# Performance work log

Measured on AMD Instinct MI355X. Metric: run time of the kernel, lower is better.

The kernel has to match this reference:

```python
import math
import jax, jax.numpy as jnp
import numpy as np

Q_MAX = 127.0  # 2**(8-1) - 1 for n_bits=8
SCALE_EPS = 1e-5


def _hadamard_matrix(n):
    H = np.array([[1.0]], dtype=np.float32)
    while H.shape[0] < n:
        H = np.block([[H, H], [H, -H]])
    return jnp.asarray(H)


def quantize_per_channel_absmax(w):
    # per output-channel absmax quantize-dequantize (torch weight per_channel)
    scales = jnp.clip(jnp.max(jnp.abs(w), axis=-1, keepdims=True) / Q_MAX, SCALE_EPS, None)
    return jnp.round(w / scales) * scales


def quantize_per_token_absmax(x):
    # per-token (last-dim) absmax quantize-dequantize
    scales = jnp.clip(jnp.max(jnp.abs(x), axis=-1, keepdims=True) / Q_MAX, SCALE_EPS, None)
    return jnp.round(x / scales) * scales


def setup_inputs() -> dict:
    key = jax.random.key(0)
    k1, k2, k3 = jax.random.split(key, 3)
    B, S, D_IN, D_OUT = 2, 2048, 4096, 4096
    x = jax.random.normal(k1, (B, S, D_IN), dtype=jnp.float32)
    # weight quantized at __init__ time (per_channel, 8-bit), as in the wrapper
    weight = quantize_per_channel_absmax(
        jax.random.normal(k2, (D_OUT, D_IN), dtype=jnp.float32) * (1.0 / math.sqrt(D_IN)))
    bias = jax.random.normal(k3, (D_OUT,), dtype=jnp.float32)
    return {"x": x, "weight": weight, "bias": bias, "had_dim": 64}


def reference(x, weight, bias, had_dim):
    # --- online_partial_had, K == 1 path ---
    B, S, D = x.shape
    n_groups = D // had_dim
    H = _hadamard_matrix(n_groups).astype(x.dtype)
    xr = x.reshape(-1, n_groups, had_dim)  # (B*S, G, had_dim)
    # hadamard_transform along the group axis, scale = 1/sqrt(G)
    xr = jnp.einsum('hg,bgd->bhd', H, xr) * (1.0 / math.sqrt(n_groups))
    x = xr.reshape(B, S, D)
    # --- per-token absmax activation quant ---
    x = quantize_per_token_absmax(x)
    # --- linear with (already quantized) weight ---
    return jnp.einsum('bsd,od->bso', x, weight) + bias
```

## Files before the change

### kernel.cpp

```cpp
#include <hip/hip_runtime.h>

#define M_DIM 4096
#define N_DIM 4096
#define K_DIM 4096

typedef __attribute__((ext_vector_type(4))) int i32x4;
typedef __attribute__((ext_vector_type(16))) int i32x16;

typedef __attribute__((address_space(1))) const void GV;
typedef __attribute__((address_space(3))) void LV;

__global__ __launch_bounds__(256) void prequant_kernel(const float* __restrict__ x,
                                                       const float* __restrict__ w,
                                                       char* __restrict__ xq,
                                                       char* __restrict__ wq,
                                                       float* __restrict__ sx,
                                                       float* __restrict__ sw) {
  const int wave = threadIdx.x >> 6;
  const int lane = threadIdx.x & 63;

  if (blockIdx.x >= 1024) {
    const int row = (blockIdx.x - 1024) * 4 + wave;
    const float* wp = w + (size_t)row * 4096;
    float4 v[16];
#pragma unroll
    for (int c = 0; c < 16; ++c) v[c] = *(const float4*)(wp + c * 256 + lane * 4);
    float amax = 0.f;
#pragma unroll
    for (int c = 0; c < 16; ++c)
      amax = fmaxf(amax, fmaxf(fmaxf(fabsf(v[c].x), fabsf(v[c].y)),
                               fmaxf(fabsf(v[c].z), fabsf(v[c].w))));
#pragma unroll
    for (int off = 32; off >= 1; off >>= 1) amax = fmaxf(amax, __shfl_xor(amax, off, 64));
    amax = fmaxf(amax, 1e-30f);
    const float inv = 127.0f / amax;
    char* op = wq + (size_t)row * 4096;
#pragma unroll
    for (int c = 0; c < 16; ++c) {
      char4 o;
      o.x = (char)rintf(v[c].x * inv);
      o.y = (char)rintf(v[c].y * inv);
      o.z = (char)rintf(v[c].z * inv);
      o.w = (char)rintf(v[c].w * inv);
      *(char4*)(op + c * 256 + lane * 4) = o;
    }
    if (lane == 0) sw[row] = amax * (1.0f / 127.0f);
    return;
  }

  const int tok = blockIdx.x * 4 + wave;
  const int gs = lane >> 4;
  const int q = lane & 15;
  const float* xp = x + (size_t)tok * 4096;

  float4 v[16];
#pragma unroll
  for (int gl = 0; gl < 16; ++gl)
    v[gl] = *(const float4*)(xp + (gl * 4 + gs) * 64 + q * 4);

#pragma unroll
  for (int s = 1; s < 16; s <<= 1) {
#pragma unroll
    for (int i = 0; i < 16; ++i) {
      if ((i & s) == 0) {
        float4 a = v[i], b = v[i | s];
        v[i].x = a.x + b.x; v[i].y = a.y + b.y; v[i].z = a.z + b.z; v[i].w = a.w + b.w;
        v[i | s].x = a.x - b.x; v[i | s].y = a.y - b.y;
        v[i | s].z = a.z - b.z; v[i | s].w = a.w - b.w;
      }
    }
  }
#pragma unroll
  for (int st = 0; st < 2; ++st) {
    const int L = 16 << st;
    const bool hi = (lane & L) != 0;
#pragma unroll
    for (int i = 0; i < 16; ++i) {
      float4 t;
      t.x = __shfl_xor(v[i].x, L, 64);
      t.y = __shfl_xor(v[i].y, L, 64);
      t.z = __shfl_xor(v[i].z, L, 64);
      t.w = __shfl_xor(v[i].w, L, 64);
      if (hi) {
        v[i].x = t.x - v[i].x; v[i].y = t.y - v[i].y;
        v[i].z = t.z - v[i].z; v[i].w = t.w - v[i].w;
      } else {
        v[i].x += t.x; v[i].y += t.y; v[i].z += t.z; v[i].w += t.w;
      }
    }
  }

  float amax = 0.f;
#pragma unroll
  for (int i = 0; i < 16; ++i) {
    v[i].x *= 0.125f; v[i].y *= 0.125f; v[i].z *= 0.125f; v[i].w *= 0.125f;
    amax = fmaxf(amax, fmaxf(fmaxf(fabsf(v[i].x), fabsf(v[i].y)),
                             fmaxf(fabsf(v[i].z), fabsf(v[i].w))));
  }
#pragma unroll
  for (int off = 32; off >= 1; off >>= 1) amax = fmaxf(amax, __shfl_xor(amax, off, 64));

  const float s = fmaxf(amax * (1.0f / 127.0f), 1e-5f);
  const float inv = 1.0f / s;

  char* op = xq + (size_t)tok * 4096;
#pragma unroll
  for (int gl = 0; gl < 16; ++gl) {
    char4 o;
    o.x = (char)rintf(v[gl].x * inv);
    o.y = (char)rintf(v[gl].y * inv);
    o.z = (char)rintf(v[gl].z * inv);
    o.w = (char)rintf(v[gl].w * inv);
    *(char4*)(op + (gl * 4 + gs) * 64 + q * 4) = o;
  }
  if (lane == 0) sx[tok] = s;
}

__global__ __launch_bounds__(512, 2) void gemm_i8(const char* __restrict__ A,
                                                  const char* __restrict__ B,
                                                  const float* __restrict__ sx,
                                                  const float* __restrict__ sw,
                                                  const float* __restrict__ bias,
                                                  float* __restrict__ C) {
  __shared__ __align__(16) char sm[65536];

  const int tid = threadIdx.x;
  const int lane = tid & 63;
  const int wave = tid >> 6;
  const int wm = wave >> 2;
  const int wn = wave & 3;
  const int m32 = lane & 31;
  const int half = lane >> 5;

  const int bid = blockIdx.x;
  const int cx = bid & 7, ii = bid >> 3;
  const int bm = (cx & 3) * 4 + (ii >> 3);
  const int bn = (cx >> 2) * 8 + (ii & 7);

  const int strow = tid >> 1;
  const int stseg = ((tid & 1) ^ ((tid >> 3) & 1)) << 4;
  const char* gA = A + (size_t)(bm * 256 + strow) * K_DIM + stseg;
  const char* gB = B + (size_t)(bn * 256 + strow) * K_DIM + stseg;

  auto lof = [&](int row) { return row * 32 + ((half ^ ((row >> 2) & 1)) << 4); };
  const int aoff0 = lof(wm * 128 + 0 + m32);
  const int aoff1 = lof(wm * 128 + 32 + m32);
  const int aoff2 = lof(wm * 128 + 64 + m32);
  const int aoff3 = lof(wm * 128 + 96 + m32);
  const int boff0 = 8192 + lof(wn * 64 + 0 + m32);
  const int boff1 = 8192 + lof(wn * 64 + 32 + m32);

  i32x16 acc[4][2];
#pragma unroll
  for (int i = 0; i < 4; ++i)
#pragma unroll
    for (int j = 0; j < 2; ++j)
#pragma unroll
      for (int r = 0; r < 16; ++r) acc[i][j][r] = 0;

#pragma unroll
  for (int s = 0; s < 3; ++s) {
    char* ld = sm + s * 16384 + (tid << 4);
    const size_t ko = (size_t)s * 32;
    __builtin_amdgcn_global_load_lds((GV*)(gA + ko), (LV*)ld, 16, 0, 0);
    __builtin_amdgcn_global_load_lds((GV*)(gB + ko), (LV*)(ld + 8192), 16, 0, 0);
  }
  asm volatile("s_waitcnt vmcnt(4)" ::: "memory");
  __builtin_amdgcn_s_barrier();

#define KTILE(T, DOSTAGE, TAILWAIT)                                                   \
  {                                                                                   \
    const char* bufp = sm + ((T) & 3) * 16384;                                        \
    if (DOSTAGE) {                                                                    \
      char* ld = sm + (((T) + 3) & 3) * 16384 + (tid << 4);                           \
      const size_t ko = (size_t)((T) + 3) * 32;                                       \
      __builtin_amdgcn_global_load_lds((GV*)(gA + ko), (LV*)ld, 16, 0, 0);            \
      __builtin_amdgcn_global_load_lds((GV*)(gB + ko), (LV*)(ld + 8192), 16, 0, 0);   \
    }                                                                                 \
    const i32x4 a0 = *(const i32x4*)(bufp + aoff0);                                   \
    const i32x4 a1 = *(const i32x4*)(bufp + aoff1);                                   \
    const i32x4 a2 = *(const i32x4*)(bufp + aoff2);                                   \
    const i32x4 a3 = *(const i32x4*)(bufp + aoff3);                                   \
    const i32x4 b0 = *(const i32x4*)(bufp + boff0);                                   \
    const i32x4 b1 = *(const i32x4*)(bufp + boff1);                                   \
    __builtin_amdgcn_s_barrier();                                                     \
    asm volatile("s_waitcnt lgkmcnt(0)" ::: "memory");                                \
    __builtin_amdgcn_sched_barrier(0);                                                \
    __builtin_amdgcn_s_setprio(1);                                                    \
    acc[0][0] = __builtin_amdgcn_mfma_i32_32x32x32_i8(a0, b0, acc[0][0], 0, 0, 0);    \
    acc[0][1] = __builtin_amdgcn_mfma_i32_32x32x32_i8(a0, b1, acc[0][1], 0, 0, 0);    \
    acc[1][0] = __builtin_amdgcn_mfma_i32_32x32x32_i8(a1, b0, acc[1][0], 0, 0, 0);    \
    acc[1][1] = __builtin_amdgcn_mfma_i32_32x32x32_i8(a1, b1, acc[1][1], 0, 0, 0);    \
    acc[2][0] = __builtin_amdgcn_mfma_i32_32x32x32_i8(a2, b0, acc[2][0], 0, 0, 0);    \
    acc[2][1] = __builtin_amdgcn_mfma_i32_32x32x32_i8(a2, b1, acc[2][1], 0, 0, 0);    \
    acc[3][0] = __builtin_amdgcn_mfma_i32_32x32x32_i8(a3, b0, acc[3][0], 0, 0, 0);    \
    acc[3][1] = __builtin_amdgcn_mfma_i32_32x32x32_i8(a3, b1, acc[3][1], 0, 0, 0);    \
    __builtin_amdgcn_s_setprio(0);                                                    \
    asm volatile("s_waitcnt " TAILWAIT ::: "memory");                                 \
    __builtin_amdgcn_s_barrier();                                                     \
  }

#pragma unroll 1
  for (int t = 0; t < 125; ++t) {
    KTILE(t, 1, "vmcnt(4)");
  }
  KTILE(125, 0, "vmcnt(2)");
  KTILE(126, 0, "vmcnt(0)");
  KTILE(127, 0, "vmcnt(0)");
#undef KTILE

  const int col0 = bn * 256 + wn * 64 + m32;
  const float swv0 = sw[col0];
  const float swv1 = sw[col0 + 32];
  const float bv0 = bias[col0];
  const float bv1 = bias[col0 + 32];

#pragma unroll
  for (int fm = 0; fm < 4; ++fm) {
    const int rbase = bm * 256 + wm * 128 + fm * 32 + 4 * half;
    float sxv[16];
#pragma unroll
    for (int r = 0; r < 16; ++r) sxv[r] = sx[rbase + (r & 3) + 8 * (r >> 2)];
#pragma unroll
    for (int fn = 0; fn < 2; ++fn) {
      const int colg = col0 + fn * 32;
      const float swb = fn ? swv1 : swv0;
      const float bvb = fn ? bv1 : bv0;
#pragma unroll
      for (int r = 0; r < 16; ++r) {
        const int rowg = rbase + (r & 3) + 8 * (r >> 2);
        C[(size_t)rowg * N_DIM + colg] = (float)acc[fm][fn][r] * (sxv[r] * swb) + bvb;
      }
    }
  }
}

extern "C" void kernel_launch(void* const* d_in, const int* in_sizes, int n_in,
                              void* d_out, int out_size, void* d_ws, size_t ws_size,
                              hipStream_t stream) {
  const float* x = (const float*)d_in[0];
  const float* w = (const float*)d_in[1];
  const float* bias = (const float*)d_in[2];

  char* xq = (char*)d_ws;
  char* wq = xq + (size_t)M_DIM * K_DIM;
  float* sx = (float*)(wq + (size_t)N_DIM * K_DIM);
  float* sw = sx + M_DIM;
  float* out = (float*)d_out;

  prequant_kernel<<<2048, 256, 0, stream>>>(x, w, xq, wq, sx, sw);

  gemm_i8<<<dim3(256), dim3(512), 0, stream>>>(xq, wq, sx, sw, bias, out);
}
```

Before: 258.8 us.

## Restructure int8 GEMM main loop to double-buffered 128-wide K tiles with phased staging

```diff
diff --git a/kernel.cpp b/kernel.cpp
--- a/kernel.cpp
+++ b/kernel.cpp
@@ -122,7 +122,7 @@
                                                   const float* __restrict__ sw,
                                                   const float* __restrict__ bias,
                                                   float* __restrict__ C) {
-  __shared__ __align__(16) char sm[65536];
+  __shared__ __align__(16) char sm[131072];
 
   const int tid = threadIdx.x;
   const int lane = tid & 63;
@@ -137,18 +137,33 @@
   const int bm = (cx & 3) * 4 + (ii >> 3);
   const int bn = (cx >> 2) * 8 + (ii & 7);
 
-  const int strow = tid >> 1;
-  const int stseg = ((tid & 1) ^ ((tid >> 3) & 1)) << 4;
-  const char* gA = A + (size_t)(bm * 256 + strow) * K_DIM + stseg;
-  const char* gB = B + (size_t)(bn * 256 + strow) * K_DIM + stseg;
-
-  auto lof = [&](int row) { return row * 32 + ((half ^ ((row >> 2) & 1)) << 4); };
-  const int aoff0 = lof(wm * 128 + 0 + m32);
-  const int aoff1 = lof(wm * 128 + 32 + m32);
-  const int aoff2 = lof(wm * 128 + 64 + m32);
-  const int aoff3 = lof(wm * 128 + 96 + m32);
-  const int boff0 = 8192 + lof(wn * 64 + 0 + m32);
-  const int boff1 = 8192 + lof(wn * 64 + 32 + m32);
+  const int r = tid >> 3;
+  const int goff = ((tid & 7) ^ (r & 7)) << 4;
+  const char* gA0 = A + (size_t)(bm * 256 + r) * K_DIM + goff;
+  const char* gB0 = B + (size_t)(bn * 256 + ((r >> 5) << 6) + (r & 31)) * K_DIM + goff;
+
+#define STAGE_A(BB, H, KO)                                                                     \
+  {                                                                                            \
+    char* d_ = sm + (BB) + (H)*16384 + (tid << 4);                                             \
+    __builtin_amdgcn_global_load_lds((GV*)(gA0 + (size_t)(H)*64 * K_DIM + (KO)), (LV*)d_, 16,  \
+                                     0, 0);                                                    \
+    __builtin_amdgcn_global_load_lds((GV*)(gA0 + (size_t)(H)*64 * K_DIM + 128 * K_DIM + (KO)), \
+                                     (LV*)(d_ + 8192), 16, 0, 0);                              \
+  }
+#define STAGE_B(BB, H, KO)                                                                     \
+  {                                                                                            \
+    char* d_ = sm + (BB) + 32768 + (H)*16384 + (tid << 4);                                     \
+    __builtin_amdgcn_global_load_lds((GV*)(gB0 + (size_t)(H)*32 * K_DIM + (KO)), (LV*)d_, 16,  \
+                                     0, 0);                                                    \
+    __builtin_amdgcn_global_load_lds((GV*)(gB0 + (size_t)(H)*32 * K_DIM + 128 * K_DIM + (KO)), \
+                                     (LV*)(d_ + 8192), 16, 0, 0);                              \
+  }
+
+  const int aRow = (wm * 64 + m32) * 128;
+  const int bRow = 32768 + (wn * 32 + m32) * 128;
+  int sl[4];
+#pragma unroll
+  for (int kc = 0; kc < 4; ++kc) sl[kc] = ((kc * 2 + half) ^ (m32 & 7)) << 4;
 
   i32x16 acc[4][2];
 #pragma unroll
@@ -156,58 +171,63 @@
 #pragma unroll
     for (int j = 0; j < 2; ++j)
 #pragma unroll
-      for (int r = 0; r < 16; ++r) acc[i][j][r] = 0;
-
-#pragma unroll
-  for (int s = 0; s < 3; ++s) {
-    char* ld = sm + s * 16384 + (tid << 4);
-    const size_t ko = (size_t)s * 32;
-    __builtin_amdgcn_global_load_lds((GV*)(gA + ko), (LV*)ld, 16, 0, 0);
-    __builtin_amdgcn_global_load_lds((GV*)(gB + ko), (LV*)(ld + 8192), 16, 0, 0);
-  }
+      for (int rr = 0; rr < 16; ++rr) acc[i][j][rr] = 0;
+
+#define PHASE(BB, MH, NH, STAGEBODY, WAITSTR)                                                  \
+  {                                                                                            \
+    const char* ap_ = sm + (BB) + (MH)*16384 + aRow;                                           \
+    const char* bp_ = sm + (BB) + (NH)*16384 + bRow;                                           \
+    i32x4 af[2][4], bf[4];                                                                     \
+    _Pragma("unroll") for (int kc = 0; kc < 4; ++kc) {                                         \
+      af[0][kc] = *(const i32x4*)(ap_ + sl[kc]);                                               \
+      af[1][kc] = *(const i32x4*)(ap_ + 4096 + sl[kc]);                                        \
+      bf[kc] = *(const i32x4*)(bp_ + sl[kc]);                                                  \
+    }                                                                                          \
+    STAGEBODY;                                                                                 \
+    asm volatile("s_waitcnt lgkmcnt(8)" ::: "memory");                                         \
+    asm volatile("s_waitcnt " WAITSTR ::: "memory");                                           \
+    __builtin_amdgcn_s_barrier();                                                              \
+    asm volatile("s_waitcnt lgkmcnt(0)" ::: "memory");                                         \
+    __builtin_amdgcn_s_setprio(1);                                                             \
+    _Pragma("unroll") for (int kc = 0; kc < 4; ++kc) {                                         \
+      acc[(MH)*2 + 0][NH] =                                                                    \
+          __builtin_amdgcn_mfma_i32_32x32x32_i8(af[0][kc], bf[kc], acc[(MH)*2 + 0][NH], 0, 0,  \
+                                                0);                                            \
+      acc[(MH)*2 + 1][NH] =                                                                    \
+          __builtin_amdgcn_mfma_i32_32x32x32_i8(af[1][kc], bf[kc], acc[(MH)*2 + 1][NH], 0, 0,  \
+                                                0);                                            \
+    }                                                                                          \
+    __builtin_amdgcn_s_setprio(0);                                                             \
+    __builtin_amdgcn_s_barrier();                                                              \
+  }
+
+  STAGE_A(0, 0, 0);
+  STAGE_B(0, 0, 0);
+  STAGE_B(0, 1, 0);
+  STAGE_A(0, 1, 0);
   asm volatile("s_waitcnt vmcnt(4)" ::: "memory");
   __builtin_amdgcn_s_barrier();
 
-#define KTILE(T, DOSTAGE, TAILWAIT)                                                   \
-  {                                                                                   \
-    const char* bufp = sm + ((T) & 3) * 16384;                                        \
-    if (DOSTAGE) {                                                                    \
-      char* ld = sm + (((T) + 3) & 3) * 16384 + (tid << 4);                           \
-      const size_t ko = (size_t)((T) + 3) * 32;                                       \
-      __builtin_amdgcn_global_load_lds((GV*)(gA + ko), (LV*)ld, 16, 0, 0);            \
-      __builtin_amdgcn_global_load_lds((GV*)(gB + ko), (LV*)(ld + 8192), 16, 0, 0);   \
-    }                                                                                 \
-    const i32x4 a0 = *(const i32x4*)(bufp + aoff0);                                   \
-    const i32x4 a1 = *(const i32x4*)(bufp + aoff1);                                   \
-    const i32x4 a2 = *(const i32x4*)(bufp + aoff2);                                   \
-    const i32x4 a3 = *(const i32x4*)(bufp + aoff3);                                   \
-    const i32x4 b0 = *(const i32x4*)(bufp + boff0);                                   \
-    const i32x4 b1 = *(const i32x4*)(bufp + boff1);                                   \
-    __builtin_amdgcn_s_barrier();                                                     \
-    asm volatile("s_waitcnt lgkmcnt(0)" ::: "memory");                                \
-    __builtin_amdgcn_sched_barrier(0);                                                \
-    __builtin_amdgcn_s_setprio(1);                                                    \
-    acc[0][0] = __builtin_amdgcn_mfma_i32_32x32x32_i8(a0, b0, acc[0][0], 0, 0, 0);    \
-    acc[0][1] = __builtin_amdgcn_mfma_i32_32x32x32_i8(a0, b1, acc[0][1], 0, 0, 0);    \
-    acc[1][0] = __builtin_amdgcn_mfma_i32_32x32x32_i8(a1, b0, acc[1][0], 0, 0, 0);    \
-    acc[1][1] = __builtin_amdgcn_mfma_i32_32x32x32_i8(a1, b1, acc[1][1], 0, 0, 0);    \
-    acc[2][0] = __builtin_amdgcn_mfma_i32_32x32x32_i8(a2, b0, acc[2][0], 0, 0, 0);    \
-    acc[2][1] = __builtin_amdgcn_mfma_i32_32x32x32_i8(a2, b1, acc[2][1], 0, 0, 0);    \
-    acc[3][0] = __builtin_amdgcn_mfma_i32_32x32x32_i8(a3, b0, acc[3][0], 0, 0, 0);    \
-    acc[3][1] = __builtin_amdgcn_mfma_i32_32x32x32_i8(a3, b1, acc[3][1], 0, 0, 0);    \
-    __builtin_amdgcn_s_setprio(0);                                                    \
-    asm volatile("s_waitcnt " TAILWAIT ::: "memory");                                 \
-    __builtin_amdgcn_s_barrier();                                                     \
-  }
-
 #pragma unroll 1
-  for (int t = 0; t < 125; ++t) {
-    KTILE(t, 1, "vmcnt(4)");
-  }
-  KTILE(125, 0, "vmcnt(2)");
-  KTILE(126, 0, "vmcnt(0)");
-  KTILE(127, 0, "vmcnt(0)");
-#undef KTILE
+  for (int t = 0; t < 31; ++t) {
+    const int BB = (t & 1) << 16;
+    const int SB = ((t + 1) & 1) << 16;
+    const int ko = (t + 1) * 128;
+    PHASE(BB, 0, 0, STAGE_A(SB, 0, ko), "vmcnt(4)");
+    PHASE(BB, 0, 1, STAGE_B(SB, 0, ko), "vmcnt(4)");
+    PHASE(BB, 1, 0, STAGE_B(SB, 1, ko), "vmcnt(4)");
+    PHASE(BB, 1, 1, STAGE_A(SB, 1, ko), "vmcnt(4)");
+  }
+  {
+    const int BB = 1 << 16;
+    PHASE(BB, 0, 0, , "vmcnt(2)");
+    PHASE(BB, 0, 1, , "vmcnt(0)");
+    PHASE(BB, 1, 0, , "vmcnt(0)");
+    PHASE(BB, 1, 1, , "vmcnt(0)");
+  }
+#undef PHASE
+#undef STAGE_A
+#undef STAGE_B
 
   const int col0 = bn * 256 + wn * 64 + m32;
   const float swv0 = sw[col0];
@@ -220,16 +240,16 @@
     const int rbase = bm * 256 + wm * 128 + fm * 32 + 4 * half;
     float sxv[16];
 #pragma unroll
-    for (int r = 0; r < 16; ++r) sxv[r] = sx[rbase + (r & 3) + 8 * (r >> 2)];
+    for (int rr = 0; rr < 16; ++rr) sxv[rr] = sx[rbase + (rr & 3) + 8 * (rr >> 2)];
 #pragma unroll
     for (int fn = 0; fn < 2; ++fn) {
       const int colg = col0 + fn * 32;
       const float swb = fn ? swv1 : swv0;
       const float bvb = fn ? bv1 : bv0;
 #pragma unroll
-      for (int r = 0; r < 16; ++r) {
-        const int rowg = rbase + (r & 3) + 8 * (r >> 2);
-        C[(size_t)rowg * N_DIM + colg] = (float)acc[fm][fn][r] * (sxv[r] * swb) + bvb;
+      for (int rr = 0; rr < 16; ++rr) {
+        const int rowg = rbase + (rr & 3) + 8 * (rr >> 2);
+        C[(size_t)rowg * N_DIM + colg] = (float)acc[fm][fn][rr] * (sxv[rr] * swb) + bvb;
       }
     }
   }
```

Result: no change. 257.2 us (-0.6%).

## Double K-tile depth to 64 with triple-buffered LDS pipeline in int8 GEMM

Applied to the files above, without the earlier changes.

```diff
diff --git a/kernel.cpp b/kernel.cpp
--- a/kernel.cpp
+++ b/kernel.cpp
@@ -122,7 +122,7 @@
                                                   const float* __restrict__ sw,
                                                   const float* __restrict__ bias,
                                                   float* __restrict__ C) {
-  __shared__ __align__(16) char sm[65536];
+  __shared__ __align__(16) char sm[98304];
 
   const int tid = threadIdx.x;
   const int lane = tid & 63;
@@ -137,18 +137,27 @@
   const int bm = (cx & 3) * 4 + (ii >> 3);
   const int bn = (cx >> 2) * 8 + (ii & 7);
 
-  const int strow = tid >> 1;
-  const int stseg = ((tid & 1) ^ ((tid >> 3) & 1)) << 4;
-  const char* gA = A + (size_t)(bm * 256 + strow) * K_DIM + stseg;
-  const char* gB = B + (size_t)(bn * 256 + strow) * K_DIM + stseg;
-
-  auto lof = [&](int row) { return row * 32 + ((half ^ ((row >> 2) & 1)) << 4); };
-  const int aoff0 = lof(wm * 128 + 0 + m32);
-  const int aoff1 = lof(wm * 128 + 32 + m32);
-  const int aoff2 = lof(wm * 128 + 64 + m32);
-  const int aoff3 = lof(wm * 128 + 96 + m32);
-  const int boff0 = 8192 + lof(wn * 64 + 0 + m32);
-  const int boff1 = 8192 + lof(wn * 64 + 32 + m32);
+  const int strow = tid >> 2;
+  const int sseg = ((tid & 3) ^ ((tid >> 3) & 3)) << 4;
+  const char* gA0 = A + (size_t)(bm * 256 + strow) * K_DIM + sseg;
+  const char* gB0 = B + (size_t)(bn * 256 + strow) * K_DIM + sseg;
+
+#define STAGE(BUFOFF, KO)                                                                \
+  {                                                                                      \
+    char* d_ = sm + (BUFOFF) + (tid << 4);                                               \
+    __builtin_amdgcn_global_load_lds((GV*)(gA0 + (KO)), (LV*)d_, 16, 0, 0);              \
+    __builtin_amdgcn_global_load_lds((GV*)(gA0 + 128 * (size_t)K_DIM + (KO)),            \
+                                     (LV*)(d_ + 8192), 16, 0, 0);                        \
+    __builtin_amdgcn_global_load_lds((GV*)(gB0 + (KO)), (LV*)(d_ + 16384), 16, 0, 0);    \
+    __builtin_amdgcn_global_load_lds((GV*)(gB0 + 128 * (size_t)K_DIM + (KO)),            \
+                                     (LV*)(d_ + 24576), 16, 0, 0);                       \
+  }
+
+  const int aBase = (wm * 128 + m32) * 64;
+  const int bBase = 16384 + (wn * 64 + m32) * 64;
+  int sl[2];
+#pragma unroll
+  for (int kc = 0; kc < 2; ++kc) sl[kc] = ((kc * 2 + half) ^ ((m32 >> 1) & 3)) << 4;
 
   i32x16 acc[4][2];
 #pragma unroll
@@ -158,56 +167,54 @@
 #pragma unroll
       for (int r = 0; r < 16; ++r) acc[i][j][r] = 0;
 
-#pragma unroll
-  for (int s = 0; s < 3; ++s) {
-    char* ld = sm + s * 16384 + (tid << 4);
-    const size_t ko = (size_t)s * 32;
-    __builtin_amdgcn_global_load_lds((GV*)(gA + ko), (LV*)ld, 16, 0, 0);
-    __builtin_amdgcn_global_load_lds((GV*)(gB + ko), (LV*)(ld + 8192), 16, 0, 0);
-  }
+  STAGE(0, 0);
+  STAGE(32768, 64);
   asm volatile("s_waitcnt vmcnt(4)" ::: "memory");
   __builtin_amdgcn_s_barrier();
-
-#define KTILE(T, DOSTAGE, TAILWAIT)                                                   \
-  {                                                                                   \
-    const char* bufp = sm + ((T) & 3) * 16384;                                        \
-    if (DOSTAGE) {                                                                    \
-      char* ld = sm + (((T) + 3) & 3) * 16384 + (tid << 4);                           \
-      const size_t ko = (size_t)((T) + 3) * 32;                                       \
-      __builtin_amdgcn_global_load_lds((GV*)(gA + ko), (LV*)ld, 16, 0, 0);            \
-      __builtin_amdgcn_global_load_lds((GV*)(gB + ko), (LV*)(ld + 8192), 16, 0, 0);   \
-    }                                                                                 \
-    const i32x4 a0 = *(const i32x4*)(bufp + aoff0);                                   \
-    const i32x4 a1 = *(const i32x4*)(bufp + aoff1);                                   \
-    const i32x4 a2 = *(const i32x4*)(bufp + aoff2);                                   \
-    const i32x4 a3 = *(const i32x4*)(bufp + aoff3);                                   \
-    const i32x4 b0 = *(const i32x4*)(bufp + boff0);                                   \
-    const i32x4 b1 = *(const i32x4*)(bufp + boff1);                                   \
-    __builtin_amdgcn_s_barrier();                                                     \
-    asm volatile("s_waitcnt lgkmcnt(0)" ::: "memory");                                \
-    __builtin_amdgcn_sched_barrier(0);                                                \
-    __builtin_amdgcn_s_setprio(1);                                                    \
-    acc[0][0] = __builtin_amdgcn_mfma_i32_32x32x32_i8(a0, b0, acc[0][0], 0, 0, 0);    \
-    acc[0][1] = __builtin_amdgcn_mfma_i32_32x32x32_i8(a0, b1, acc[0][1], 0, 0, 0);    \
-    acc[1][0] = __builtin_amdgcn_mfma_i32_32x32x32_i8(a1, b0, acc[1][0], 0, 0, 0);    \
-    acc[1][1] = __builtin_amdgcn_mfma_i32_32x32x32_i8(a1, b1, acc[1][1], 0, 0, 0);    \
-    acc[2][0] = __builtin_amdgcn_mfma_i32_32x32x32_i8(a2, b0, acc[2][0], 0, 0, 0);    \
-    acc[2][1] = __builtin_amdgcn_mfma_i32_32x32x32_i8(a2, b1, acc[2][1], 0, 0, 0);    \
-    acc[3][0] = __builtin_amdgcn_mfma_i32_32x32x32_i8(a3, b0, acc[3][0], 0, 0, 0);    \
-    acc[3][1] = __builtin_amdgcn_mfma_i32_32x32x32_i8(a3, b1, acc[3][1], 0, 0, 0);    \
-    __builtin_amdgcn_s_setprio(0);                                                    \
-    asm volatile("s_waitcnt " TAILWAIT ::: "memory");                                 \
-    __builtin_amdgcn_s_barrier();                                                     \
-  }
+  __builtin_amdgcn_sched_barrier(0);
+
+  int o0 = 0, o1 = 32768, o2 = 65536;
 
 #pragma unroll 1
-  for (int t = 0; t < 125; ++t) {
-    KTILE(t, 1, "vmcnt(4)");
-  }
-  KTILE(125, 0, "vmcnt(2)");
-  KTILE(126, 0, "vmcnt(0)");
-  KTILE(127, 0, "vmcnt(0)");
-#undef KTILE
+  for (int t = 0; t < 64; ++t) {
+    const char* bufp = sm + o0;
+
+    i32x4 af[2][4], bf[2][2];
+#pragma unroll
+    for (int kc = 0; kc < 2; ++kc) {
+#pragma unroll
+      for (int fm = 0; fm < 4; ++fm)
+        af[kc][fm] = *(const i32x4*)(bufp + aBase + fm * 2048 + sl[kc]);
+#pragma unroll
+      for (int fn = 0; fn < 2; ++fn)
+        bf[kc][fn] = *(const i32x4*)(bufp + bBase + fn * 2048 + sl[kc]);
+    }
+
+    if (t < 62) STAGE(o2, (size_t)(t + 2) * 64);
+
+    __builtin_amdgcn_s_setprio(1);
+#pragma unroll
+    for (int kc = 0; kc < 2; ++kc)
+#pragma unroll
+      for (int fm = 0; fm < 4; ++fm)
+#pragma unroll
+        for (int fn = 0; fn < 2; ++fn)
+          acc[fm][fn] =
+              __builtin_amdgcn_mfma_i32_32x32x32_i8(af[kc][fm], bf[kc][fn], acc[fm][fn], 0, 0, 0);
+    __builtin_amdgcn_s_setprio(0);
+
+    if (t < 62) {
+      asm volatile("s_waitcnt vmcnt(4)" ::: "memory");
+    } else if (t == 62) {
+      asm volatile("s_waitcnt vmcnt(0)" ::: "memory");
+    }
+    if (t < 63) {
+      __builtin_amdgcn_s_barrier();
+      __builtin_amdgcn_sched_barrier(0);
+    }
+    const int tmp = o0; o0 = o1; o1 = o2; o2 = tmp;
+  }
+#undef STAGE
 
   const int col0 = bn * 256 + wn * 64 + m32;
   const float swv0 = sw[col0];
```

Result: faster. 244.1 us (-5.7%).
